# Kernel optimization log

Measured on AMD Instinct MI355X. Metric: run time of the kernel, lower is better.

Reference implementation:

```python
import jax, jax.numpy as jnp
import numpy as np

NUM_FEATURES = 81   # atom feature width used in matmuls
N_NODES = 262144
N_COLS = 103        # num_features + num_bond
OUT_CH = 128
COORD = 3           # distance rule slice [0:3]


def setup_inputs() -> dict:
    key = jax.random.key(0)
    k1, k2, k3, k4 = jax.random.split(key, 4)
    features = jax.random.normal(k1, (N_NODES, N_COLS), dtype=jnp.float32)
    # columns 81, 82 hold neighbor indices (0 => no neighbor), stored as floats
    idx = jax.random.randint(k4, (N_NODES, 2), 0, N_NODES).astype(jnp.float32)
    features = features.at[:, NUM_FEATURES:NUM_FEATURES + 2].set(idx)
    w_s = jax.random.normal(k2, (NUM_FEATURES, OUT_CH), dtype=jnp.float32) * 0.05
    w_n = jax.random.normal(k3, (N_COLS, OUT_CH), dtype=jnp.float32) * 0.05
    return {"features": features, "w_s": w_s, "w_n": w_n}


def reference(features, w_s, w_n):
    F = NUM_FEATURES
    self_f = features[:, :F]                       # [N, F]
    new_features = self_f @ w_s                    # [N, C] self term

    idx0 = features[:, F].astype(jnp.int32)        # neighbor slot 0
    idx1 = features[:, F + 1].astype(jnp.int32)    # neighbor slot 1

    def neighbor_contrib(idx):
        nei = features[idx]                                        # gather [N, 103]
        # rule 0: 'distance' over [0:COORD] -> keep neighbor slice, record distance
        d = jnp.sqrt(jnp.sum(jnp.square(self_f[:, :COORD] - nei[:, :COORD]), axis=-1))
        seg_dist = nei[:, :COORD]                                  # [N, 3]
        # rule 1: 'sum' over [COORD:F]
        seg_sum = self_f[:, COORD:F] + nei[:, COORD:F]             # [N, F-3]
        comb = jnp.concatenate([seg_dist, seg_sum], axis=-1)       # [N, F]
        d_eff = jnp.where(d > 0, d, jnp.float32(0.01))
        comb = comb / jnp.square(d_eff)[:, None]                   # distance scaling
        return comb @ w_n[:F] + new_features                       # tiny-matmul batched

    c0 = neighbor_contrib(idx0)
    c1 = neighbor_contrib(idx1)
    # rows with no valid neighbor were never written -> zeros
    out = jnp.where((idx1 != 0)[:, None], c1,
                    jnp.where((idx0 != 0)[:, None], c0, jnp.float32(0.0)))
    return out
```

## Files before the change

### kernel.cpp

```cpp
#include <hip/hip_runtime.h>
#include <hip/hip_bf16.h>

constexpr int kNodes = 262144;
constexpr int NC  = 103;
constexpr int F   = 81;
constexpr int OC  = 128;
constexpr int NKS = 6;
constexpr int NPB = 64;
constexpr int THREADS = 256;
constexpr int NEI_STRIDE = 100;
constexpr int GW = 96;

typedef __attribute__((ext_vector_type(8))) short bf16x8;
typedef __attribute__((ext_vector_type(4))) float f32x4;

__device__ inline ushort f2bf(float f) {
  uint u = __float_as_uint(f);
  return (ushort)((u + 0x7fffu + ((u >> 16) & 1u)) >> 16);
}

__device__ inline short bfc(float x) {
  return (short)__bfloat16_as_ushort(__float2bfloat16(x));
}

__global__ __launch_bounds__(256)
void prep_w(const float* __restrict__ w_s, const float* __restrict__ w_n,
            ushort* __restrict__ wf) {
  int t = blockIdx.x * 256 + threadIdx.x;
  if (t >= NKS * 8 * 64) return;
  int l  = t & 63;
  int ct = (t >> 6) & 7;
  int ks = t >> 9;
  int c  = ct * 16 + (l & 15);
  int kb = ks * 32 + ((l >> 4) << 3);
  union { ushort u[8]; int4 v; } o;
  #pragma unroll
  for (int i = 0; i < 8; ++i) {
    int k = kb + i;
    float f = 0.f;
    if (k < F)                      f = w_s[k * OC + c];
    else if (k >= 96 && k < 96 + F) f = w_n[(k - 96) * OC + c];
    o.u[i] = f2bf(f);
  }
  ((int4*)wf)[t] = o.v;
}

__global__ __launch_bounds__(THREADS)
void rgc_v8(const float* __restrict__ feat, const ushort* __restrict__ wf,
            float* __restrict__ out) {
  __shared__ float lds_self[NPB * NC];
  __shared__ float lds_nei[NPB * NEI_STRIDE];
  __shared__ int   s_sel[NPB];
  __shared__ float s_alive[NPB];
  __shared__ float s_cs[NPB];

  const int tid = threadIdx.x;
  const int w   = tid >> 6;
  const int l   = tid & 63;
  const long base = (long)blockIdx.x * NPB;
  const float* fbase = feat + base * NC;

  const bf16x8* wfv = (const bf16x8*)wf;
  bf16x8 bA[NKS], bB[NKS];
  #pragma unroll
  for (int ks = 0; ks < NKS; ++ks) {
    bA[ks] = wfv[(ks * 8 + w)     * 64 + l];
    bB[ks] = wfv[(ks * 8 + w + 4) * 64 + l];
  }

  {
    const float4* src = (const float4*)fbase;
    float4* dst = (float4*)lds_self;
    #pragma unroll
    for (int i = tid; i < NPB * NC / 4; i += THREADS) dst[i] = src[i];
  }
  __syncthreads();

  if (tid < NPB) {
    int n = tid;
    int i0 = (int)lds_self[n * NC + F];
    int i1 = (int)lds_self[n * NC + F + 1];
    s_sel[n]   = (i1 != 0) ? i1 : i0;
    s_alive[n] = (i1 != 0 || i0 != 0) ? 1.f : 0.f;
  }
  __syncthreads();

  #pragma unroll
  for (int j = 0; j < 24; ++j) {
    int v   = tid + j * THREADS;
    int row = v / GW;
    int col = v - row * GW;
    lds_nei[row * NEI_STRIDE + col] = feat[(long)s_sel[row] * NC + col];
  }
  __syncthreads();

  if (tid < NPB) {
    int n = tid;
    float dx = lds_self[n * NC + 0] - lds_nei[n * NEI_STRIDE + 0];
    float dy = lds_self[n * NC + 1] - lds_nei[n * NEI_STRIDE + 1];
    float dz = lds_self[n * NC + 2] - lds_nei[n * NEI_STRIDE + 2];
    float d2 = dx * dx + dy * dy + dz * dz;
    s_cs[n] = s_alive[n] * ((d2 > 0.f) ? (1.f / d2) : 10000.f);
  }
  __syncthreads();

  const int q    = l >> 4;
  const int lrow = l & 15;
  const int off0 = q * 8;
  const int col  = l & 15;

  #pragma unroll
  for (int nt = 0; nt < 4; ++nt) {
    const int n = nt * 16 + lrow;
    const float* sp = lds_self + n * NC;
    const float* np = lds_nei + n * NEI_STRIDE;
    const float alive = s_alive[n];
    const float cs    = s_cs[n];

    bf16x8 afS[3], afC[3];
    #pragma unroll
    for (int c = 0; c < 3; ++c) {
      #pragma unroll
      for (int i = 0; i < 8; ++i) {
        float sv = sp[c * 32 + off0 + i];
        float nv = np[c * 32 + off0 + i];
        afS[c][i] = bfc(sv * alive);
        float se = sv;
        if (c == 0 && i < 3 && q == 0) se = 0.f;
        afC[c][i] = bfc((nv + se) * cs);
      }
    }

    f32x4 a0 = (f32x4)(0.f), a1 = (f32x4)(0.f);
    #pragma unroll
    for (int ks = 0; ks < NKS; ++ks) {
      bf16x8 af = (ks < 3) ? afS[ks] : afC[ks - 3];
      a0 = __builtin_amdgcn_mfma_f32_16x16x32_bf16(af, bA[ks], a0, 0, 0, 0);
      a1 = __builtin_amdgcn_mfma_f32_16x16x32_bf16(af, bB[ks], a1, 0, 0, 0);
    }

    const long orow = base + nt * 16 + q * 4;
    #pragma unroll
    for (int r = 0; r < 4; ++r) {
      out[(orow + r) * OC + w * 16       + col] = a0[r];
      out[(orow + r) * OC + (w + 4) * 16 + col] = a1[r];
    }
  }
}

extern "C" void kernel_launch(void* const* d_in, const int* in_sizes, int n_in,
                              void* d_out, int out_size, void* d_ws, size_t ws_size,
                              hipStream_t stream) {
  const float* feat = (const float*)d_in[0];
  const float* w_s  = (const float*)d_in[1];
  const float* w_n  = (const float*)d_in[2];
  float* outp = (float*)d_out;
  ushort* wf = (ushort*)d_ws;

  prep_w<<<dim3((NKS * 8 * 64 + 255) / 256), 256, 0, stream>>>(w_s, w_n, wf);
  rgc_v8<<<dim3(kNodes / NPB), THREADS, 0, stream>>>(feat, wf, outp);
}
```

Baseline: 67.91 us.

## Process four node tiles per block with register-staged prefetch of next tile

Each block now handles four 64-node tiles instead of one. Global loads for the next tile's self rows and gathered neighbor rows are issued into registers before the current tile's MFMA work, so memory latency overlaps with compute. The selection index and distance scale are computed up front per thread directly from global memory, which removes two barrier phases. This costs more VGPRs for the staging buffers and launches a quarter as many blocks, which may lower occupancy and parallelism.

```diff
diff --git a/kernel.cpp b/kernel.cpp
--- a/kernel.cpp
+++ b/kernel.cpp
@@ -7,9 +7,11 @@
 constexpr int OC  = 128;
 constexpr int NKS = 6;
 constexpr int NPB = 64;
+constexpr int TPB = 4;
 constexpr int THREADS = 256;
 constexpr int NEI_STRIDE = 100;
 constexpr int GW = 96;
+constexpr int SELF_F4 = NPB * NC / 4;
 
 typedef __attribute__((ext_vector_type(8))) short bf16x8;
 typedef __attribute__((ext_vector_type(4))) float f32x4;
@@ -18,7 +20,6 @@
   uint u = __float_as_uint(f);
   return (ushort)((u + 0x7fffu + ((u >> 16) & 1u)) >> 16);
 }
-
 __device__ inline short bfc(float x) {
   return (short)__bfloat16_as_ushort(__float2bfloat16(x));
 }
@@ -46,19 +47,17 @@
 }
 
 __global__ __launch_bounds__(THREADS)
-void rgc_v8(const float* __restrict__ feat, const ushort* __restrict__ wf,
+void rgc_v9(const float* __restrict__ feat, const ushort* __restrict__ wf,
             float* __restrict__ out) {
-  __shared__ float lds_self[NPB * NC];
-  __shared__ float lds_nei[NPB * NEI_STRIDE];
-  __shared__ int   s_sel[NPB];
-  __shared__ float s_alive[NPB];
-  __shared__ float s_cs[NPB];
+  __shared__ __align__(16) float lds_self[NPB * NC];
+  __shared__ __align__(16) float lds_nei[NPB * NEI_STRIDE];
+  __shared__ int   s_sel[THREADS];
+  __shared__ float s_cs[THREADS];
 
   const int tid = threadIdx.x;
   const int w   = tid >> 6;
   const int l   = tid & 63;
-  const long base = (long)blockIdx.x * NPB;
-  const float* fbase = feat + base * NC;
+  const long bbase = (long)blockIdx.x * (NPB * TPB);
 
   const bf16x8* wfv = (const bf16x8*)wf;
   bf16x8 bA[NKS], bB[NKS];
@@ -69,83 +68,108 @@
   }
 
   {
-    const float4* src = (const float4*)fbase;
-    float4* dst = (float4*)lds_self;
-    #pragma unroll
-    for (int i = tid; i < NPB * NC / 4; i += THREADS) dst[i] = src[i];
+    const float* row = feat + (bbase + tid) * NC;
+    float f0 = row[F], f1 = row[F + 1];
+    int i0 = (int)f0, i1 = (int)f1;
+    int sel = (i1 != 0) ? i1 : i0;
+    const float* nr = feat + (long)sel * NC;
+    float dx = row[0] - nr[0];
+    float dy = row[1] - nr[1];
+    float dz = row[2] - nr[2];
+    float d2 = dx * dx + dy * dy + dz * dz;
+    float alive = (sel != 0) ? 1.f : 0.f;
+    s_sel[tid] = sel;
+    s_cs[tid]  = alive * ((d2 > 0.f) ? (1.f / d2) : 10000.f);
   }
   __syncthreads();
 
-  if (tid < NPB) {
-    int n = tid;
-    int i0 = (int)lds_self[n * NC + F];
-    int i1 = (int)lds_self[n * NC + F + 1];
-    s_sel[n]   = (i1 != 0) ? i1 : i0;
-    s_alive[n] = (i1 != 0 || i0 != 0) ? 1.f : 0.f;
+  f32x4 st[7];
+  f32x4 ng[6];
+
+#define STAGE(T)                                                            \
+  {                                                                         \
+    const f32x4* src = (const f32x4*)(feat + (bbase + (long)(T) * NPB) * NC); \
+    _Pragma("unroll")                                                       \
+    for (int j = 0; j < 6; ++j) st[j] = src[tid + j * THREADS];             \
+    if (tid < SELF_F4 - 6 * THREADS) st[6] = src[tid + 6 * THREADS];        \
+    _Pragma("unroll")                                                       \
+    for (int j = 0; j < 24; ++j) {                                          \
+      int v = tid + j * THREADS;                                            \
+      int r = v / GW;                                                       \
+      int c = v - r * GW;                                                   \
+      ng[j >> 2][j & 3] = feat[(long)s_sel[(T) * NPB + r] * NC + c];        \
+    }                                                                       \
+    asm volatile("" :: "v"(st[0]), "v"(st[1]), "v"(st[2]), "v"(st[3]),      \
+                       "v"(st[4]), "v"(st[5]), "v"(st[6]));                 \
+    asm volatile("" :: "v"(ng[0]), "v"(ng[1]), "v"(ng[2]), "v"(ng[3]),      \
+                       "v"(ng[4]), "v"(ng[5]));                             \
   }
-  __syncthreads();
 
-  #pragma unroll
-  for (int j = 0; j < 24; ++j) {
-    int v   = tid + j * THREADS;
-    int row = v / GW;
-    int col = v - row * GW;
-    lds_nei[row * NEI_STRIDE + col] = feat[(long)s_sel[row] * NC + col];
-  }
-  __syncthreads();
-
-  if (tid < NPB) {
-    int n = tid;
-    float dx = lds_self[n * NC + 0] - lds_nei[n * NEI_STRIDE + 0];
-    float dy = lds_self[n * NC + 1] - lds_nei[n * NEI_STRIDE + 1];
-    float dz = lds_self[n * NC + 2] - lds_nei[n * NEI_STRIDE + 2];
-    float d2 = dx * dx + dy * dy + dz * dz;
-    s_cs[n] = s_alive[n] * ((d2 > 0.f) ? (1.f / d2) : 10000.f);
-  }
-  __syncthreads();
+  STAGE(0);
 
   const int q    = l >> 4;
   const int lrow = l & 15;
   const int off0 = q * 8;
   const int col  = l & 15;
 
-  #pragma unroll
-  for (int nt = 0; nt < 4; ++nt) {
-    const int n = nt * 16 + lrow;
-    const float* sp = lds_self + n * NC;
-    const float* np = lds_nei + n * NEI_STRIDE;
-    const float alive = s_alive[n];
-    const float cs    = s_cs[n];
-
-    bf16x8 afS[3], afC[3];
-    #pragma unroll
-    for (int c = 0; c < 3; ++c) {
+  for (int t = 0; t < TPB; ++t) {
+    {
+      f32x4* dst = (f32x4*)lds_self;
       #pragma unroll
-      for (int i = 0; i < 8; ++i) {
-        float sv = sp[c * 32 + off0 + i];
-        float nv = np[c * 32 + off0 + i];
-        afS[c][i] = bfc(sv * alive);
-        float se = sv;
-        if (c == 0 && i < 3 && q == 0) se = 0.f;
-        afC[c][i] = bfc((nv + se) * cs);
+      for (int j = 0; j < 6; ++j) dst[tid + j * THREADS] = st[j];
+      if (tid < SELF_F4 - 6 * THREADS) dst[tid + 6 * THREADS] = st[6];
+      #pragma unroll
+      for (int j = 0; j < 24; ++j) {
+        int v = tid + j * THREADS;
+        int r = v / GW;
+        int c = v - r * GW;
+        lds_nei[r * NEI_STRIDE + c] = ng[j >> 2][j & 3];
       }
     }
+    __syncthreads();
 
-    f32x4 a0 = (f32x4)(0.f), a1 = (f32x4)(0.f);
+    if (t + 1 < TPB) STAGE(t + 1);
+
     #pragma unroll
-    for (int ks = 0; ks < NKS; ++ks) {
-      bf16x8 af = (ks < 3) ? afS[ks] : afC[ks - 3];
-      a0 = __builtin_amdgcn_mfma_f32_16x16x32_bf16(af, bA[ks], a0, 0, 0, 0);
-      a1 = __builtin_amdgcn_mfma_f32_16x16x32_bf16(af, bB[ks], a1, 0, 0, 0);
+    for (int nt = 0; nt < 4; ++nt) {
+      const int n = nt * 16 + lrow;
+      const float* sp = lds_self + n * NC;
+      const float* np = lds_nei + n * NEI_STRIDE;
+      const float alive = (s_sel[t * NPB + n] != 0) ? 1.f : 0.f;
+      const float cs    = s_cs[t * NPB + n];
+
+      bf16x8 afS[3], afC[3];
+      #pragma unroll
+      for (int c = 0; c < 3; ++c) {
+        #pragma unroll
+        for (int i = 0; i < 8; ++i) {
+          float sv = sp[c * 32 + off0 + i];
+          float nv = np[c * 32 + off0 + i];
+          afS[c][i] = bfc(sv * alive);
+          float se = sv;
+          if (c == 0 && i < 3 && q == 0) se = 0.f;
+          afC[c][i] = bfc((nv + se) * cs);
+        }
+      }
+
+      f32x4 a0 = (f32x4)(0.f), a1 = (f32x4)(0.f);
+      #pragma unroll
+      for (int ks = 0; ks < NKS; ++ks) {
+        bf16x8 af = (ks < 3) ? afS[ks] : afC[ks - 3];
+        a0 = __builtin_amdgcn_mfma_f32_16x16x32_bf16(af, bA[ks], a0, 0, 0, 0);
+        a1 = __builtin_amdgcn_mfma_f32_16x16x32_bf16(af, bB[ks], a1, 0, 0, 0);
+      }
+
+      const long orow = bbase + t * NPB + nt * 16 + q * 4;
+      #pragma unroll
+      for (int r = 0; r < 4; ++r) {
+        out[(orow + r) * OC + w * 16       + col] = a0[r];
+        out[(orow + r) * OC + (w + 4) * 16 + col] = a1[r];
+      }
     }
-
-    const long orow = base + nt * 16 + q * 4;
-    #pragma unroll
-    for (int r = 0; r < 4; ++r) {
-      out[(orow + r) * OC + w * 16       + col] = a0[r];
-      out[(orow + r) * OC + (w + 4) * 16 + col] = a1[r];
-    }
+    __syncthreads();
   }
+#undef STAGE
 }
 
 extern "C" void kernel_launch(void* const* d_in, const int* in_sizes, int n_in,
@@ -158,5 +182,5 @@
   ushort* wf = (ushort*)d_ws;
 
   prep_w<<<dim3((NKS * 8 * 64 + 255) / 256), 256, 0, stream>>>(w_s, w_n, wf);
-  rgc_v8<<<dim3(kNodes / NPB), THREADS, 0, stream>>>(feat, wf, outp);
+  rgc_v9<<<dim3(kNodes / (NPB * TPB)), THREADS, 0, stream>>>(feat, wf, outp);
 }
```

Measured after the change: 89.09 us. 1.31x slower.

## Stage bf16 A-operand in LDS and compute distance scale directly from global

Applied to the files above, without the earlier changes.

Replaces the fp32 self and neighbor LDS staging with a single bf16 A-matrix tile in LDS. The self and combined-neighbor operands are precomputed and packed by the load loops, so the MFMA loop reads ready bf16x8 vectors instead of converting per element. Per-row distance and selection are now computed straight from global memory, which removes two barriers. The alive mask moves to the output multiply, and occupancy is raised via launch bounds. Global loads become 2-float strided accesses instead of float4 coalesced copies, which may hurt memory efficiency.

```diff
diff --git a/kernel.cpp b/kernel.cpp
--- a/kernel.cpp
+++ b/kernel.cpp
@@ -8,8 +8,7 @@
 constexpr int NKS = 6;
 constexpr int NPB = 64;
 constexpr int THREADS = 256;
-constexpr int NEI_STRIDE = 100;
-constexpr int GW = 96;
+constexpr int AST = 200;
 
 typedef __attribute__((ext_vector_type(8))) short bf16x8;
 typedef __attribute__((ext_vector_type(4))) float f32x4;
@@ -18,9 +17,10 @@
   uint u = __float_as_uint(f);
   return (ushort)((u + 0x7fffu + ((u >> 16) & 1u)) >> 16);
 }
-
-__device__ inline short bfc(float x) {
-  return (short)__bfloat16_as_ushort(__float2bfloat16(x));
+__device__ inline uint pk2(float a, float b) {
+  ushort ua = __bfloat16_as_ushort(__float2bfloat16(a));
+  ushort ub = __bfloat16_as_ushort(__float2bfloat16(b));
+  return (uint)ua | ((uint)ub << 16);
 }
 
 __global__ __launch_bounds__(256)
@@ -45,20 +45,17 @@
   ((int4*)wf)[t] = o.v;
 }
 
-__global__ __launch_bounds__(THREADS)
-void rgc_v8(const float* __restrict__ feat, const ushort* __restrict__ wf,
-            float* __restrict__ out) {
-  __shared__ float lds_self[NPB * NC];
-  __shared__ float lds_nei[NPB * NEI_STRIDE];
+__global__ __launch_bounds__(THREADS, 4)
+void rgc_v10(const float* __restrict__ feat, const ushort* __restrict__ wf,
+             float* __restrict__ out) {
+  __shared__ __align__(16) ushort a_bf[NPB * AST];
   __shared__ int   s_sel[NPB];
-  __shared__ float s_alive[NPB];
   __shared__ float s_cs[NPB];
 
   const int tid = threadIdx.x;
   const int w   = tid >> 6;
   const int l   = tid & 63;
   const long base = (long)blockIdx.x * NPB;
-  const float* fbase = feat + base * NC;
 
   const bf16x8* wfv = (const bf16x8*)wf;
   bf16x8 bA[NKS], bB[NKS];
@@ -68,82 +65,76 @@
     bB[ks] = wfv[(ks * 8 + w + 4) * 64 + l];
   }
 
-  {
-    const float4* src = (const float4*)fbase;
-    float4* dst = (float4*)lds_self;
-    #pragma unroll
-    for (int i = tid; i < NPB * NC / 4; i += THREADS) dst[i] = src[i];
+  if (l < 16) {
+    const int n = w * 16 + l;
+    const float* row = feat + (base + n) * NC;
+    float f0 = row[F], f1 = row[F + 1];
+    int i0 = (int)f0, i1 = (int)f1;
+    int sel = (i1 != 0) ? i1 : i0;
+    const float* nr = feat + (long)sel * NC;
+    float dx = row[0] - nr[0];
+    float dy = row[1] - nr[1];
+    float dz = row[2] - nr[2];
+    float d2 = dx * dx + dy * dy + dz * dz;
+    float alive = (sel != 0) ? 1.f : 0.f;
+    s_sel[n] = sel;
+    s_cs[n]  = alive * ((d2 > 0.f) ? (1.f / d2) : 10000.f);
   }
-  __syncthreads();
-
-  if (tid < NPB) {
-    int n = tid;
-    int i0 = (int)lds_self[n * NC + F];
-    int i1 = (int)lds_self[n * NC + F + 1];
-    s_sel[n]   = (i1 != 0) ? i1 : i0;
-    s_alive[n] = (i1 != 0 || i0 != 0) ? 1.f : 0.f;
+  #pragma unroll
+  for (int j = 0; j < 12; ++j) {
+    int v  = tid + j * THREADS;
+    int n  = v / 48;
+    int kp = (v - n * 48) * 2;
+    const float* sr = feat + (base + n) * NC + kp;
+    float x0 = sr[0], x1 = sr[1];
+    *(uint*)&a_bf[n * AST + kp] = pk2(x0, x1);
   }
   __syncthreads();
 
   #pragma unroll
-  for (int j = 0; j < 24; ++j) {
-    int v   = tid + j * THREADS;
-    int row = v / GW;
-    int col = v - row * GW;
-    lds_nei[row * NEI_STRIDE + col] = feat[(long)s_sel[row] * NC + col];
-  }
-  __syncthreads();
-
-  if (tid < NPB) {
-    int n = tid;
-    float dx = lds_self[n * NC + 0] - lds_nei[n * NEI_STRIDE + 0];
-    float dy = lds_self[n * NC + 1] - lds_nei[n * NEI_STRIDE + 1];
-    float dz = lds_self[n * NC + 2] - lds_nei[n * NEI_STRIDE + 2];
-    float d2 = dx * dx + dy * dy + dz * dz;
-    s_cs[n] = s_alive[n] * ((d2 > 0.f) ? (1.f / d2) : 10000.f);
+  for (int j = 0; j < 12; ++j) {
+    int v  = tid + j * THREADS;
+    int n  = v / 48;
+    int kp = (v - n * 48) * 2;
+    const float* nr = feat + (long)s_sel[n] * NC + kp;
+    const float* sr = feat + (base + n) * NC + kp;
+    float cs = s_cs[n];
+    float nv0 = nr[0], nv1 = nr[1];
+    float sv0 = sr[0], sv1 = sr[1];
+    float y0 = (nv0 + ((kp     < 3) ? 0.f : sv0)) * cs;
+    float y1 = (nv1 + ((kp + 1 < 3) ? 0.f : sv1)) * cs;
+    *(uint*)&a_bf[n * AST + 96 + kp] = pk2(y0, y1);
   }
   __syncthreads();
 
   const int q    = l >> 4;
   const int lrow = l & 15;
-  const int off0 = q * 8;
   const int col  = l & 15;
 
   #pragma unroll
   for (int nt = 0; nt < 4; ++nt) {
-    const int n = nt * 16 + lrow;
-    const float* sp = lds_self + n * NC;
-    const float* np = lds_nei + n * NEI_STRIDE;
-    const float alive = s_alive[n];
-    const float cs    = s_cs[n];
-
-    bf16x8 afS[3], afC[3];
+    const ushort* ap = a_bf + (nt * 16 + lrow) * AST + q * 8;
+    bf16x8 af[NKS];
     #pragma unroll
-    for (int c = 0; c < 3; ++c) {
-      #pragma unroll
-      for (int i = 0; i < 8; ++i) {
-        float sv = sp[c * 32 + off0 + i];
-        float nv = np[c * 32 + off0 + i];
-        afS[c][i] = bfc(sv * alive);
-        float se = sv;
-        if (c == 0 && i < 3 && q == 0) se = 0.f;
-        afC[c][i] = bfc((nv + se) * cs);
-      }
-    }
+    for (int ks = 0; ks < NKS; ++ks) af[ks] = *(const bf16x8*)(ap + ks * 32);
 
     f32x4 a0 = (f32x4)(0.f), a1 = (f32x4)(0.f);
     #pragma unroll
     for (int ks = 0; ks < NKS; ++ks) {
-      bf16x8 af = (ks < 3) ? afS[ks] : afC[ks - 3];
-      a0 = __builtin_amdgcn_mfma_f32_16x16x32_bf16(af, bA[ks], a0, 0, 0, 0);
-      a1 = __builtin_amdgcn_mfma_f32_16x16x32_bf16(af, bB[ks], a1, 0, 0, 0);
+      a0 = __builtin_amdgcn_mfma_f32_16x16x32_bf16(af[ks], bA[ks], a0, 0, 0, 0);
+      a1 = __builtin_amdgcn_mfma_f32_16x16x32_bf16(af[ks], bB[ks], a1, 0, 0, 0);
     }
+
+    float al[4];
+    #pragma unroll
+    for (int r = 0; r < 4; ++r)
+      al[r] = (s_sel[nt * 16 + q * 4 + r] != 0) ? 1.f : 0.f;
 
     const long orow = base + nt * 16 + q * 4;
     #pragma unroll
     for (int r = 0; r < 4; ++r) {
-      out[(orow + r) * OC + w * 16       + col] = a0[r];
-      out[(orow + r) * OC + (w + 4) * 16 + col] = a1[r];
+      out[(orow + r) * OC + w * 16       + col] = a0[r] * al[r];
+      out[(orow + r) * OC + (w + 4) * 16 + col] = a1[r] * al[r];
     }
   }
 }
@@ -158,5 +149,5 @@
   ushort* wf = (ushort*)d_ws;
 
   prep_w<<<dim3((NKS * 8 * 64 + 255) / 256), 256, 0, stream>>>(w_s, w_n, wf);
-  rgc_v8<<<dim3(kNodes / NPB), THREADS, 0, stream>>>(feat, wf, outp);
+  rgc_v10<<<dim3(kNodes / NPB), THREADS, 0, stream>>>(feat, wf, outp);
 }
```

Result: slower. 144.8 us (+113.2%).
